# Optimization experiments

Hardware: AMD Instinct MI355X
Metric: run time of the kernel (lower is better)

The kernel has to match this reference:

```python
import jax, jax.numpy as jnp
import numpy as np
from jax.ops import segment_sum

N = 100000
E = 1600000


def gcn_conv(x, W, b, src, dst, n_nodes):
    # PyG GCNConv: linear transform, then symmetric-normalized scatter-add.
    # src/dst already include self-loops; edge weights are all ones.
    h = x @ W  # [N, out]
    deg = segment_sum(jnp.ones(src.shape[0], dtype=x.dtype), dst, num_segments=n_nodes)
    dinv = jnp.where(deg > 0, jax.lax.rsqrt(jnp.maximum(deg, 1e-12)), 0.0).astype(x.dtype)
    norm = dinv[src] * dinv[dst]  # [E]
    msg = h[src] * norm[:, None]  # gather + scale, [E, out]
    out = segment_sum(msg, dst, num_segments=n_nodes)  # scatter-add
    return out + b


def setup_inputs() -> dict:
    key = jax.random.key(0)
    k1, k2, k3, k4 = jax.random.split(key, 4)
    x = jax.random.normal(k1, (N, 128), dtype=jnp.float32)
    edge_index = jax.random.randint(k2, (2, E), 0, N, dtype=jnp.int32)
    # Glorot-ish scaled weights
    W1 = jax.random.normal(k3, (128, 64), dtype=jnp.float32) * (1.0 / np.sqrt(128))
    b1 = jnp.zeros((64,), dtype=jnp.float32)
    W2 = jax.random.normal(k4, (64, 32), dtype=jnp.float32) * (1.0 / np.sqrt(64))
    b2 = jnp.zeros((32,), dtype=jnp.float32)
    return {"x": x, "edge_index": edge_index, "W1": W1, "b1": b1, "W2": W2, "b2": b2}


def reference(x, edge_index, W1, b1, W2, b2):
    n = x.shape[0]
    # add self-loops (PyG default add_self_loops=True)
    loops = jnp.arange(n, dtype=edge_index.dtype)
    src = jnp.concatenate([edge_index[0], loops])
    dst = jnp.concatenate([edge_index[1], loops])
    h = gcn_conv(x, W1, b1, src, dst, n)
    h = jax.nn.relu(h)
    out = gcn_conv(h, W2, b2, src, dst, n)
    return out
```

## Files before the change

kernel.cpp:

```cpp
#include <hip/hip_runtime.h>
#include <hip/hip_fp16.h>

#define BS 256
#define BSHIFT 9
#define BNODES (1 << BSHIFT)
#define NB 256
#define CHUNK 4096

typedef _Float16 f16x8 __attribute__((ext_vector_type(8)));
typedef float f32x4 __attribute__((ext_vector_type(4)));


__global__ __launch_bounds__(BS) void k_count(const int* __restrict__ dst,
                                              int* __restrict__ bucketCount, int E) {
    __shared__ int h[NB];
    int t = threadIdx.x;
    h[t] = 0;
    __syncthreads();
    int base = blockIdx.x * CHUNK;
#pragma unroll
    for (int j = 0; j < CHUNK / BS; ++j) {
        int e = base + j * BS + t;
        if (e < E) atomicAdd(&h[dst[e] >> BSHIFT], 1);
    }
    __syncthreads();
    if (h[t]) atomicAdd(&bucketCount[t], h[t]);
}

__global__ void k_bucket_scan(const int* __restrict__ bucketCount,
                              int* __restrict__ bucketBase,
                              int* __restrict__ gcursor) {
    int t = threadIdx.x;
    int v = bucketCount[t];
    int incl = v;
    int lane = t & 63, w = t >> 6;
#pragma unroll
    for (int off = 1; off < 64; off <<= 1) {
        int u = __shfl_up(incl, off);
        if (lane >= off) incl += u;
    }
    __shared__ int ws[4];
    if (lane == 63) ws[w] = incl;
    __syncthreads();
    int woff = 0;
    for (int q = 0; q < w; ++q) woff += ws[q];
    int excl = woff + incl - v;
    bucketBase[t] = excl;
    gcursor[t] = excl;
    if (t == NB - 1) bucketBase[NB] = excl + v;
}

__global__ __launch_bounds__(BS) void k_scatter(const int* __restrict__ src,
                                                const int* __restrict__ dst,
                                                int* __restrict__ gcursor,
                                                int2* __restrict__ binned, int E) {
    __shared__ int h[NB];
    __shared__ int base[NB];
    int t = threadIdx.x;
    h[t] = 0;
    __syncthreads();
    int cbase = blockIdx.x * CHUNK;
    int sv[CHUNK / BS], dv[CHUNK / BS], rv[CHUNK / BS];
#pragma unroll
    for (int j = 0; j < CHUNK / BS; ++j) {
        int e = cbase + j * BS + t;
        rv[j] = -1;
        if (e < E) {
            sv[j] = src[e];
            dv[j] = dst[e];
            rv[j] = atomicAdd(&h[dv[j] >> BSHIFT], 1);
        }
    }
    __syncthreads();
    base[t] = h[t] ? atomicAdd(&gcursor[t], h[t]) : 0;
    __syncthreads();
#pragma unroll
    for (int j = 0; j < CHUNK / BS; ++j) {
        if (rv[j] >= 0) {
            int b = dv[j] >> BSHIFT;
            binned[base[b] + rv[j]] = make_int2(sv[j], dv[j]);
        }
    }
}

__global__ __launch_bounds__(BS) void k_b1(const int2* __restrict__ binned,
                                           const int* __restrict__ bucketBase,
                                           int* __restrict__ deg, int n) {
    __shared__ int h[BNODES];
    int t = threadIdx.x;
    int node0 = blockIdx.x << BSHIFT;
    int nn = min(BNODES, n - node0);
#pragma unroll
    for (int i = t; i < BNODES; i += BS) h[i] = 0;
    __syncthreads();
    int eb = bucketBase[blockIdx.x], ee = bucketBase[blockIdx.x + 1];
    for (int e = eb + t; e < ee; e += BS) {
        int d = binned[e].y;
        atomicAdd(&h[d - node0], 1);
    }
    __syncthreads();
    for (int i = t; i < nn; i += BS) deg[node0 + i] = h[i] + 1;
}


__global__ void k_block_sums(const int* __restrict__ deg, int* __restrict__ bsum, int n) {
    int t = threadIdx.x;
    int base = blockIdx.x * (BS * 8) + t * 8;
    int s = 0;
#pragma unroll
    for (int j = 0; j < 8; ++j) {
        int i = base + j;
        if (i < n) s += deg[i];
    }
#pragma unroll
    for (int off = 32; off > 0; off >>= 1) s += __shfl_down(s, off);
    __shared__ int ws[BS / 64];
    int lane = t & 63, w = t >> 6;
    if (lane == 0) ws[w] = s;
    __syncthreads();
    if (t == 0) {
        int tot = 0;
        for (int q = 0; q < BS / 64; ++q) tot += ws[q];
        bsum[blockIdx.x] = tot;
    }
}

__global__ void k_spine(const int* __restrict__ bsum, int* __restrict__ boff,
                        int* __restrict__ total_out, int nb) {
    int t = threadIdx.x;
    int v = (t < nb) ? bsum[t] : 0;
    int incl = v;
#pragma unroll
    for (int off = 1; off < 64; off <<= 1) {
        int u = __shfl_up(incl, off);
        if (t >= off) incl += u;
    }
    if (t < nb) boff[t] = incl - v;
    if (t == 63) *total_out = incl;
}

__global__ void k_scan_final(const int* __restrict__ deg, const int* __restrict__ boff,
                             int* __restrict__ rowptr, float* __restrict__ dinv, int n) {
    int t = threadIdx.x;
    int base = blockIdx.x * (BS * 8) + t * 8;
    int epre[8];
    int run = 0;
#pragma unroll
    for (int j = 0; j < 8; ++j) {
        epre[j] = run;
        int i = base + j;
        if (i < n) run += deg[i];
    }
    int lane = t & 63, w = t >> 6;
    int incl = run;
#pragma unroll
    for (int off = 1; off < 64; off <<= 1) {
        int u = __shfl_up(incl, off);
        if (lane >= off) incl += u;
    }
    __shared__ int ws[BS / 64];
    if (lane == 63) ws[w] = incl;
    __syncthreads();
    int woff = 0;
    for (int q = 0; q < w; ++q) woff += ws[q];
    int texcl = boff[blockIdx.x] + woff + (incl - run);
#pragma unroll
    for (int j = 0; j < 8; ++j) {
        int i = base + j;
        if (i < n) {
            rowptr[i] = texcl + epre[j];
            dinv[i] = rsqrtf((float)deg[i]);
        }
    }
}

__global__ __launch_bounds__(BS) void k_b2(const int2* __restrict__ binned,
                                           const int* __restrict__ bucketBase,
                                           const int* __restrict__ rowptr,
                                           int* __restrict__ csr, int n) {
    __shared__ int rp[BNODES];
    __shared__ int cur[BNODES];
    int t = threadIdx.x;
    int node0 = blockIdx.x << BSHIFT;
    int nn = min(BNODES, n - node0);
#pragma unroll
    for (int i = t; i < BNODES; i += BS) cur[i] = 1;
    for (int i = t; i < nn; i += BS) {
        int r = rowptr[node0 + i];
        rp[i] = r;
        csr[r] = node0 + i;
    }
    __syncthreads();
    int eb = bucketBase[blockIdx.x], ee = bucketBase[blockIdx.x + 1];
    for (int e = eb + t; e < ee; e += BS) {
        int2 p = binned[e];
        int li = p.y - node0;
        int r = atomicAdd(&cur[li], 1);
        csr[rp[li] + r] = p.x;
    }
}


template <int K, int COLS, bool FUSE, bool IN_HALF>
__global__ __launch_bounds__(BS, 4) void k_mgemm(const void* __restrict__ Xv,
                                                 const float* __restrict__ W,
                                                 const float* __restrict__ bias,
                                                 const float* __restrict__ dscale,
                                                 __half* __restrict__ H, int n) {
    constexpr int KC = K / 8;
    constexpr int SWZ = (KC - 1) < 15 ? (KC - 1) : 15;
    constexpr int NT = COLS / 16;
    __shared__ __align__(16) _Float16 sB[COLS * K];
    int tid = threadIdx.x;

    for (int idx = tid; idx < COLS * KC; idx += BS) {
        int c = idx / KC, k8 = idx % KC;
        f16x8 v;
#pragma unroll
        for (int j = 0; j < 8; ++j) v[j] = (_Float16)W[(k8 * 8 + j) * COLS + c];
        *(f16x8*)&sB[c * K + ((k8 ^ (c & SWZ)) * 8)] = v;
    }
    __syncthreads();

    int w = tid >> 6, lane = tid & 63;
    int lm = lane & 15, q = lane >> 4;
    int row_m0 = blockIdx.x * 128 + w * 32;

    f32x4 acc[2][NT];
#pragma unroll
    for (int tm = 0; tm < 2; ++tm)
#pragma unroll
        for (int tn = 0; tn < NT; ++tn) acc[tm][tn] = (f32x4){0.f, 0.f, 0.f, 0.f};

#pragma unroll
    for (int kk = 0; kk < K / 32; ++kk) {
        int k0 = kk * 32 + q * 8;
        f16x8 af[2], bf[NT];
#pragma unroll
        for (int tm = 0; tm < 2; ++tm) {
            int row = row_m0 + tm * 16 + lm;
            int rl = row < n ? row : (n - 1);
            if (IN_HALF) {
                f16x8 raw = *(const f16x8*)((const _Float16*)Xv + (size_t)rl * K + k0);
                if (FUSE) {
                    const float4* bp = (const float4*)(bias + k0);
                    float4 ba = bp[0], bb = bp[1];
                    float f[8] = {(float)raw[0], (float)raw[1], (float)raw[2], (float)raw[3],
                                  (float)raw[4], (float)raw[5], (float)raw[6], (float)raw[7]};
                    f[0] = fmaxf(f[0] + ba.x, 0.f); f[1] = fmaxf(f[1] + ba.y, 0.f);
                    f[2] = fmaxf(f[2] + ba.z, 0.f); f[3] = fmaxf(f[3] + ba.w, 0.f);
                    f[4] = fmaxf(f[4] + bb.x, 0.f); f[5] = fmaxf(f[5] + bb.y, 0.f);
                    f[6] = fmaxf(f[6] + bb.z, 0.f); f[7] = fmaxf(f[7] + bb.w, 0.f);
#pragma unroll
                    for (int j = 0; j < 8; ++j) raw[j] = (_Float16)f[j];
                }
                af[tm] = raw;
            } else {
                const float4* xp = (const float4*)Xv + ((size_t)rl * K + k0) / 4;
                float4 a = xp[0], b = xp[1];
                f16x8 v;
                v[0] = (_Float16)a.x; v[1] = (_Float16)a.y;
                v[2] = (_Float16)a.z; v[3] = (_Float16)a.w;
                v[4] = (_Float16)b.x; v[5] = (_Float16)b.y;
                v[6] = (_Float16)b.z; v[7] = (_Float16)b.w;
                af[tm] = v;
            }
        }
#pragma unroll
        for (int tn = 0; tn < NT; ++tn) {
            int c = tn * 16 + lm;
            bf[tn] = *(const f16x8*)&sB[c * K + (((kk * 4 + q) ^ (c & SWZ)) * 8)];
        }
#pragma unroll
        for (int tm = 0; tm < 2; ++tm)
#pragma unroll
            for (int tn = 0; tn < NT; ++tn)
                acc[tm][tn] = __builtin_amdgcn_mfma_f32_16x16x32_f16(af[tm], bf[tn],
                                                                     acc[tm][tn], 0, 0, 0);
    }

#pragma unroll
    for (int tm = 0; tm < 2; ++tm) {
#pragma unroll
        for (int r = 0; r < 4; ++r) {
            int row = row_m0 + tm * 16 + q * 4 + r;
            if (row < n) {
                float dv = dscale[row];
#pragma unroll
                for (int tn = 0; tn < NT; ++tn) {
                    int col = tn * 16 + lm;
                    H[(size_t)row * COLS + col] = __float2half_rn(acc[tm][tn][r] * dv);
                }
            }
        }
    }
}


__global__ __launch_bounds__(BS) void k_agg64(const __half* __restrict__ h,
                                              const int* __restrict__ csr,
                                              const int* __restrict__ rowptr,
                                              const float* __restrict__ dinv,
                                              __half* __restrict__ out, int n) {
    int wid = (blockIdx.x * BS + threadIdx.x) >> 6;
    int lane = threadIdx.x & 63;
    int half = lane >> 5, hl = lane & 31;
    int node = wid * 2 + half;
    bool valid = node < n;
    int b = 0, e = 0;
    if (valid) { b = rowptr[node]; e = rowptr[node + 1]; }
    int slot = hl >> 4, fq = hl & 15;
    float a0 = 0.f, a1 = 0.f, a2 = 0.f, a3 = 0.f;
    for (int c = b; c < e; c += 32) {
        int m = e - c;
        if (m > 32) m = 32;
        int sv = (hl < m) ? csr[c + hl] : 0;
        for (int j = 0; j < m; j += 2) {
            int js = j + slot;
            int s = __shfl(sv, js < m ? js : 0, 32);
            if (js < m) {
                float2 raw = *(const float2*)(h + (size_t)s * 64 + fq * 4);
                __half2 h0 = ((const __half2*)&raw)[0], h1 = ((const __half2*)&raw)[1];
                float2 f0 = __half22float2(h0), f1 = __half22float2(h1);
                a0 += f0.x; a1 += f0.y; a2 += f1.x; a3 += f1.y;
            }
        }
    }
    a0 += __shfl_down(a0, 16); a1 += __shfl_down(a1, 16);
    a2 += __shfl_down(a2, 16); a3 += __shfl_down(a3, 16);
    if (valid && hl < 16) {
        float dv = dinv[node];
        union { __half2 h2[2]; float2 f2; } pk;
        pk.h2[0] = __floats2half2_rn(a0 * dv, a1 * dv);
        pk.h2[1] = __floats2half2_rn(a2 * dv, a3 * dv);
        *(float2*)(out + (size_t)node * 64 + hl * 4) = pk.f2;
    }
}

__global__ __launch_bounds__(BS) void k_agg32(const __half* __restrict__ h,
                                              const int* __restrict__ csr,
                                              const int* __restrict__ rowptr,
                                              const float* __restrict__ dinv,
                                              const float* __restrict__ bias,
                                              float* __restrict__ out, int n) {
    int wid = (blockIdx.x * BS + threadIdx.x) >> 6;
    int lane = threadIdx.x & 63;
    int half = lane >> 5, hl = lane & 31;
    int node = wid * 2 + half;
    bool valid = node < n;
    int b = 0, e = 0;
    if (valid) { b = rowptr[node]; e = rowptr[node + 1]; }
    int slot = hl >> 3, fq = hl & 7;
    float a0 = 0.f, a1 = 0.f, a2 = 0.f, a3 = 0.f;
    for (int c = b; c < e; c += 32) {
        int m = e - c;
        if (m > 32) m = 32;
        int sv = (hl < m) ? csr[c + hl] : 0;
        for (int j = 0; j < m; j += 4) {
            int js = j + slot;
            int s = __shfl(sv, js < m ? js : 0, 32);
            if (js < m) {
                float2 raw = *(const float2*)(h + (size_t)s * 32 + fq * 4);
                __half2 h0 = ((const __half2*)&raw)[0], h1 = ((const __half2*)&raw)[1];
                float2 f0 = __half22float2(h0), f1 = __half22float2(h1);
                a0 += f0.x; a1 += f0.y; a2 += f1.x; a3 += f1.y;
            }
        }
    }
    a0 += __shfl_down(a0, 16); a1 += __shfl_down(a1, 16);
    a2 += __shfl_down(a2, 16); a3 += __shfl_down(a3, 16);
    a0 += __shfl_down(a0, 8);  a1 += __shfl_down(a1, 8);
    a2 += __shfl_down(a2, 8);  a3 += __shfl_down(a3, 8);
    if (valid && hl < 8) {
        float dv = dinv[node];
        float4 bv = ((const float4*)bias)[hl];
        float4 o = make_float4(a0 * dv + bv.x, a1 * dv + bv.y,
                               a2 * dv + bv.z, a3 * dv + bv.w);
        ((float4*)(out + (size_t)node * 32))[hl] = o;
    }
}


extern "C" void kernel_launch(void* const* d_in, const int* in_sizes, int n_in,
                              void* d_out, int out_size, void* d_ws, size_t ws_size,
                              hipStream_t stream) {
    const float* x  = (const float*)d_in[0];
    const int* eidx = (const int*)d_in[1];
    const float* W1 = (const float*)d_in[2];
    const float* b1 = (const float*)d_in[3];
    const float* W2 = (const float*)d_in[4];
    const float* b2 = (const float*)d_in[5];
    float* out = (float*)d_out;

    int n = in_sizes[0] / 128;
    int E = in_sizes[1] / 2;
    const int* srcA = eidx;
    const int* dstA = eidx + E;

    char* p = (char*)d_ws;
    auto alloc = [&](size_t bytes) {
        char* q = p;
        p += (bytes + 255) & ~(size_t)255;
        return q;
    };
    int*    deg     = (int*)alloc((size_t)n * 4);
    int*    rowptr  = (int*)alloc((size_t)(n + 1) * 4);
    int*    bsum    = (int*)alloc(64 * 4);
    int*    boff    = (int*)alloc(64 * 4);
    float*  dinv    = (float*)alloc((size_t)n * 4);
    int*    bcount  = (int*)alloc(NB * 4);
    int*    bbase   = (int*)alloc((NB + 1) * 4);
    int*    gcursor = (int*)alloc(NB * 4);
    int2*   binned  = (int2*)alloc((size_t)E * 8);
    int*    csr     = (int*)alloc((size_t)(E + n) * 4);
    __half* h1      = (__half*)alloc((size_t)n * 64 * 2);
    __half* g1      = (__half*)alloc((size_t)n * 64 * 2);
    __half* h2      = (__half*)alloc((size_t)n * 32 * 2);

    int nb_scan  = (n + BS * 8 - 1) / (BS * 8);
    int nchunks  = (E + CHUNK - 1) / CHUNK;
    int nbuckets = (n + BNODES - 1) / BNODES;
    int nblk     = (n + 127) / 128;
    int npairs   = (n + 1) / 2;
    int aggblk   = (int)(((size_t)npairs * 64 + BS - 1) / BS);

    hipMemsetAsync(bcount, 0, NB * 4, stream);
    k_count<<<nchunks, BS, 0, stream>>>(dstA, bcount, E);
    k_bucket_scan<<<1, BS, 0, stream>>>(bcount, bbase, gcursor);
    k_scatter<<<nchunks, BS, 0, stream>>>(srcA, dstA, gcursor, binned, E);
    k_b1<<<nbuckets, BS, 0, stream>>>(binned, bbase, deg, n);
    k_block_sums<<<nb_scan, BS, 0, stream>>>(deg, bsum, n);
    k_spine<<<1, 64, 0, stream>>>(bsum, boff, rowptr + n, nb_scan);
    k_scan_final<<<nb_scan, BS, 0, stream>>>(deg, boff, rowptr, dinv, n);
    k_b2<<<nbuckets, BS, 0, stream>>>(binned, bbase, rowptr, csr, n);

    k_mgemm<128, 64, false, false><<<nblk, BS, 0, stream>>>(x, W1, nullptr, dinv, h1, n);
    k_agg64<<<aggblk, BS, 0, stream>>>(h1, csr, rowptr, dinv, g1, n);

    k_mgemm<64, 32, true, true><<<nblk, BS, 0, stream>>>(g1, W2, b1, dinv, h2, n);
    k_agg32<<<aggblk, BS, 0, stream>>>(h2, csr, rowptr, dinv, b2, out, n);
}
```

Baseline: 270.6 us.

## Fuse CSR build into one per-bucket kernel, pack binned edges, unroll aggregation

Packs each binned edge into a single int (17-bit source plus 9-bit local destination), halving the binned array traffic. Five kernels (degree count, three global-scan kernels, CSR fill) are merged into one per-bucket kernel that derives row pointers from the bucket base plus a local scan, which removes launches and the global deg round trip. The aggregation loops are unrolled to issue four gathers at once into two accumulator sets to raise memory-level parallelism. The packing assumes node ids fit in 17 bits.

```diff
diff --git a/kernel.cpp b/kernel.cpp
--- a/kernel.cpp
+++ b/kernel.cpp
@@ -53,7 +53,7 @@
 __global__ __launch_bounds__(BS) void k_scatter(const int* __restrict__ src,
                                                 const int* __restrict__ dst,
                                                 int* __restrict__ gcursor,
-                                                int2* __restrict__ binned, int E) {
+                                                int* __restrict__ binned, int E) {
     __shared__ int h[NB];
     __shared__ int base[NB];
     int t = threadIdx.x;
@@ -78,125 +78,67 @@
     for (int j = 0; j < CHUNK / BS; ++j) {
         if (rv[j] >= 0) {
             int b = dv[j] >> BSHIFT;
-            binned[base[b] + rv[j]] = make_int2(sv[j], dv[j]);
-        }
-    }
-}
-
-__global__ __launch_bounds__(BS) void k_b1(const int2* __restrict__ binned,
-                                           const int* __restrict__ bucketBase,
-                                           int* __restrict__ deg, int n) {
+            binned[base[b] + rv[j]] = sv[j] | ((dv[j] & (BNODES - 1)) << 17);
+        }
+    }
+}
+
+__global__ __launch_bounds__(BS) void k_build(const int* __restrict__ binned,
+                                              const int* __restrict__ bucketBase,
+                                              int* __restrict__ rowptr,
+                                              float* __restrict__ dinv,
+                                              int* __restrict__ csr, int n, int E) {
     __shared__ int h[BNODES];
+    __shared__ int rp[BNODES];
+    __shared__ int cur[BNODES];
+    __shared__ int ws[4];
     int t = threadIdx.x;
-    int node0 = blockIdx.x << BSHIFT;
+    int bkt = blockIdx.x;
+    int node0 = bkt << BSHIFT;
     int nn = min(BNODES, n - node0);
 #pragma unroll
     for (int i = t; i < BNODES; i += BS) h[i] = 0;
     __syncthreads();
-    int eb = bucketBase[blockIdx.x], ee = bucketBase[blockIdx.x + 1];
-    for (int e = eb + t; e < ee; e += BS) {
-        int d = binned[e].y;
-        atomicAdd(&h[d - node0], 1);
-    }
-    __syncthreads();
-    for (int i = t; i < nn; i += BS) deg[node0 + i] = h[i] + 1;
-}
-
-
-__global__ void k_block_sums(const int* __restrict__ deg, int* __restrict__ bsum, int n) {
-    int t = threadIdx.x;
-    int base = blockIdx.x * (BS * 8) + t * 8;
-    int s = 0;
-#pragma unroll
-    for (int j = 0; j < 8; ++j) {
-        int i = base + j;
-        if (i < n) s += deg[i];
-    }
-#pragma unroll
-    for (int off = 32; off > 0; off >>= 1) s += __shfl_down(s, off);
-    __shared__ int ws[BS / 64];
+    int eb = bucketBase[bkt], ee = bucketBase[bkt + 1];
+    for (int e = eb + t; e < ee; e += BS)
+        atomicAdd(&h[binned[e] >> 17], 1);
+    __syncthreads();
+    int i0 = 2 * t;
+    int v0 = h[i0], v1 = h[i0 + 1];
+    int pair = v0 + v1;
     int lane = t & 63, w = t >> 6;
-    if (lane == 0) ws[w] = s;
-    __syncthreads();
-    if (t == 0) {
-        int tot = 0;
-        for (int q = 0; q < BS / 64; ++q) tot += ws[q];
-        bsum[blockIdx.x] = tot;
-    }
-}
-
-__global__ void k_spine(const int* __restrict__ bsum, int* __restrict__ boff,
-                        int* __restrict__ total_out, int nb) {
-    int t = threadIdx.x;
-    int v = (t < nb) ? bsum[t] : 0;
-    int incl = v;
-#pragma unroll
-    for (int off = 1; off < 64; off <<= 1) {
-        int u = __shfl_up(incl, off);
-        if (t >= off) incl += u;
-    }
-    if (t < nb) boff[t] = incl - v;
-    if (t == 63) *total_out = incl;
-}
-
-__global__ void k_scan_final(const int* __restrict__ deg, const int* __restrict__ boff,
-                             int* __restrict__ rowptr, float* __restrict__ dinv, int n) {
-    int t = threadIdx.x;
-    int base = blockIdx.x * (BS * 8) + t * 8;
-    int epre[8];
-    int run = 0;
-#pragma unroll
-    for (int j = 0; j < 8; ++j) {
-        epre[j] = run;
-        int i = base + j;
-        if (i < n) run += deg[i];
-    }
-    int lane = t & 63, w = t >> 6;
-    int incl = run;
+    int incl = pair;
 #pragma unroll
     for (int off = 1; off < 64; off <<= 1) {
         int u = __shfl_up(incl, off);
         if (lane >= off) incl += u;
     }
-    __shared__ int ws[BS / 64];
     if (lane == 63) ws[w] = incl;
     __syncthreads();
     int woff = 0;
     for (int q = 0; q < w; ++q) woff += ws[q];
-    int texcl = boff[blockIdx.x] + woff + (incl - run);
-#pragma unroll
-    for (int j = 0; j < 8; ++j) {
-        int i = base + j;
-        if (i < n) {
-            rowptr[i] = texcl + epre[j];
-            dinv[i] = rsqrtf((float)deg[i]);
-        }
-    }
-}
-
-__global__ __launch_bounds__(BS) void k_b2(const int2* __restrict__ binned,
-                                           const int* __restrict__ bucketBase,
-                                           const int* __restrict__ rowptr,
-                                           int* __restrict__ csr, int n) {
-    __shared__ int rp[BNODES];
-    __shared__ int cur[BNODES];
-    int t = threadIdx.x;
-    int node0 = blockIdx.x << BSHIFT;
-    int nn = min(BNODES, n - node0);
-#pragma unroll
-    for (int i = t; i < BNODES; i += BS) cur[i] = 1;
-    for (int i = t; i < nn; i += BS) {
-        int r = rowptr[node0 + i];
-        rp[i] = r;
-        csr[r] = node0 + i;
-    }
-    __syncthreads();
-    int eb = bucketBase[blockIdx.x], ee = bucketBase[blockIdx.x + 1];
+    int excl = woff + incl - pair;
+    int r0 = eb + node0 + excl + i0;
+    int r1 = r0 + v0 + 1;
+    rp[i0] = r0; rp[i0 + 1] = r1;
+    cur[i0] = 1; cur[i0 + 1] = 1;
+    if (i0 < nn) {
+        rowptr[node0 + i0] = r0;
+        dinv[node0 + i0] = rsqrtf((float)(v0 + 1));
+        csr[r0] = node0 + i0;
+    }
+    if (i0 + 1 < nn) {
+        rowptr[node0 + i0 + 1] = r1;
+        dinv[node0 + i0 + 1] = rsqrtf((float)(v1 + 1));
+        csr[r1] = node0 + i0 + 1;
+    }
+    if (bkt == 0 && t == 0) rowptr[n] = E + n;
+    __syncthreads();
     for (int e = eb + t; e < ee; e += BS) {
-        int2 p = binned[e];
-        int li = p.y - node0;
+        int p = binned[e];
+        int li = p >> 17;
         int r = atomicAdd(&cur[li], 1);
-        csr[rp[li] + r] = p.x;
+        csr[rp[li] + r] = p & 0x1FFFF;
     }
 }
 
@@ -297,6 +239,13 @@
 }
 
 
+__device__ __forceinline__ void acc_h4(float2 raw, float& x0, float& x1,
+                                       float& x2, float& x3) {
+    __half2 u0 = ((const __half2*)&raw)[0], u1 = ((const __half2*)&raw)[1];
+    float2 f0 = __half22float2(u0), f1 = __half22float2(u1);
+    x0 += f0.x; x1 += f0.y; x2 += f1.x; x3 += f1.y;
+}
+
 __global__ __launch_bounds__(BS) void k_agg64(const __half* __restrict__ h,
                                               const int* __restrict__ csr,
                                               const int* __restrict__ rowptr,
@@ -311,21 +260,36 @@
     if (valid) { b = rowptr[node]; e = rowptr[node + 1]; }
     int slot = hl >> 4, fq = hl & 15;
     float a0 = 0.f, a1 = 0.f, a2 = 0.f, a3 = 0.f;
+    float c0 = 0.f, c1 = 0.f, c2 = 0.f, c3 = 0.f;
     for (int c = b; c < e; c += 32) {
         int m = e - c;
         if (m > 32) m = 32;
         int sv = (hl < m) ? csr[c + hl] : 0;
-        for (int j = 0; j < m; j += 2) {
+        int j = 0;
+        for (; j + 7 < m; j += 8) {
+            int sA = __shfl(sv, j + slot, 32);
+            int sB = __shfl(sv, j + 2 + slot, 32);
+            int sC = __shfl(sv, j + 4 + slot, 32);
+            int sD = __shfl(sv, j + 6 + slot, 32);
+            float2 rA = *(const float2*)(h + (size_t)sA * 64 + fq * 4);
+            float2 rB = *(const float2*)(h + (size_t)sB * 64 + fq * 4);
+            float2 rC = *(const float2*)(h + (size_t)sC * 64 + fq * 4);
+            float2 rD = *(const float2*)(h + (size_t)sD * 64 + fq * 4);
+            acc_h4(rA, a0, a1, a2, a3);
+            acc_h4(rB, c0, c1, c2, c3);
+            acc_h4(rC, a0, a1, a2, a3);
+            acc_h4(rD, c0, c1, c2, c3);
+        }
+        for (; j < m; j += 2) {
             int js = j + slot;
             int s = __shfl(sv, js < m ? js : 0, 32);
             if (js < m) {
                 float2 raw = *(const float2*)(h + (size_t)s * 64 + fq * 4);
-                __half2 h0 = ((const __half2*)&raw)[0], h1 = ((const __half2*)&raw)[1];
-                float2 f0 = __half22float2(h0), f1 = __half22float2(h1);
-                a0 += f0.x; a1 += f0.y; a2 += f1.x; a3 += f1.y;
+                acc_h4(raw, a0, a1, a2, a3);
             }
         }
     }
+    a0 += c0; a1 += c1; a2 += c2; a3 += c3;
     a0 += __shfl_down(a0, 16); a1 += __shfl_down(a1, 16);
     a2 += __shfl_down(a2, 16); a3 += __shfl_down(a3, 16);
     if (valid && hl < 16) {
@@ -352,21 +316,36 @@
     if (valid) { b = rowptr[node]; e = rowptr[node + 1]; }
     int slot = hl >> 3, fq = hl & 7;
     float a0 = 0.f, a1 = 0.f, a2 = 0.f, a3 = 0.f;
+    float c0 = 0.f, c1 = 0.f, c2 = 0.f, c3 = 0.f;
     for (int c = b; c < e; c += 32) {
         int m = e - c;
         if (m > 32) m = 32;
         int sv = (hl < m) ? csr[c + hl] : 0;
-        for (int j = 0; j < m; j += 4) {
+        int j = 0;
+        for (; j + 15 < m; j += 16) {
+            int sA = __shfl(sv, j + slot, 32);
+            int sB = __shfl(sv, j + 4 + slot, 32);
+            int sC = __shfl(sv, j + 8 + slot, 32);
+            int sD = __shfl(sv, j + 12 + slot, 32);
+            float2 rA = *(const float2*)(h + (size_t)sA * 32 + fq * 4);
+            float2 rB = *(const float2*)(h + (size_t)sB * 32 + fq * 4);
+            float2 rC = *(const float2*)(h + (size_t)sC * 32 + fq * 4);
+            float2 rD = *(const float2*)(h + (size_t)sD * 32 + fq * 4);
+            acc_h4(rA, a0, a1, a2, a3);
+            acc_h4(rB, c0, c1, c2, c3);
+            acc_h4(rC, a0, a1, a2, a3);
+            acc_h4(rD, c0, c1, c2, c3);
+        }
+        for (; j < m; j += 4) {
             int js = j + slot;
             int s = __shfl(sv, js < m ? js : 0, 32);
             if (js < m) {
                 float2 raw = *(const float2*)(h + (size_t)s * 32 + fq * 4);
-                __half2 h0 = ((const __half2*)&raw)[0], h1 = ((const __half2*)&raw)[1];
-                float2 f0 = __half22float2(h0), f1 = __half22float2(h1);
-                a0 += f0.x; a1 += f0.y; a2 += f1.x; a3 += f1.y;
+                acc_h4(raw, a0, a1, a2, a3);
             }
         }
     }
+    a0 += c0; a1 += c1; a2 += c2; a3 += c3;
     a0 += __shfl_down(a0, 16); a1 += __shfl_down(a1, 16);
     a2 += __shfl_down(a2, 16); a3 += __shfl_down(a3, 16);
     a0 += __shfl_down(a0, 8);  a1 += __shfl_down(a1, 8);
@@ -403,21 +382,17 @@
         p += (bytes + 255) & ~(size_t)255;
         return q;
     };
-    int*    deg     = (int*)alloc((size_t)n * 4);
     int*    rowptr  = (int*)alloc((size_t)(n + 1) * 4);
-    int*    bsum    = (int*)alloc(64 * 4);
-    int*    boff    = (int*)alloc(64 * 4);
     float*  dinv    = (float*)alloc((size_t)n * 4);
     int*    bcount  = (int*)alloc(NB * 4);
     int*    bbase   = (int*)alloc((NB + 1) * 4);
     int*    gcursor = (int*)alloc(NB * 4);
-    int2*   binned  = (int2*)alloc((size_t)E * 8);
+    int*    binned  = (int*)alloc((size_t)E * 4);
     int*    csr     = (int*)alloc((size_t)(E + n) * 4);
     __half* h1      = (__half*)alloc((size_t)n * 64 * 2);
     __half* g1      = (__half*)alloc((size_t)n * 64 * 2);
     __half* h2      = (__half*)alloc((size_t)n * 32 * 2);
 
-    int nb_scan  = (n + BS * 8 - 1) / (BS * 8);
     int nchunks  = (E + CHUNK - 1) / CHUNK;
     int nbuckets = (n + BNODES - 1) / BNODES;
     int nblk     = (n + 127) / 128;
@@ -428,11 +403,7 @@
     k_count<<<nchunks, BS, 0, stream>>>(dstA, bcount, E);
     k_bucket_scan<<<1, BS, 0, stream>>>(bcount, bbase, gcursor);
     k_scatter<<<nchunks, BS, 0, stream>>>(srcA, dstA, gcursor, binned, E);
-    k_b1<<<nbuckets, BS, 0, stream>>>(binned, bbase, deg, n);
-    k_block_sums<<<nb_scan, BS, 0, stream>>>(deg, bsum, n);
-    k_spine<<<1, 64, 0, stream>>>(bsum, boff, rowptr + n, nb_scan);
-    k_scan_final<<<nb_scan, BS, 0, stream>>>(deg, boff, rowptr, dinv, n);
-    k_b2<<<nbuckets, BS, 0, stream>>>(binned, bbase, rowptr, csr, n);
+    k_build<<<nbuckets, BS, 0, stream>>>(binned, bbase, rowptr, dinv, csr, n, E);
 
     k_mgemm<128, 64, false, false><<<nblk, BS, 0, stream>>>(x, W1, nullptr, dinv, h1, n);
     k_agg64<<<aggblk, BS, 0, stream>>>(h1, csr, rowptr, dinv, g1, n);
```

Result: faster. 241.1 us (-10.9%).
